# Performance work log

Hardware: AMD Instinct MI355X
Metric: run time of the kernel (lower is better)

Reference implementation:

```python
import jax, jax.numpy as jnp
import numpy as np

jax.config.update("jax_enable_x64", True)

QN = 20       # number of qubits -> statevector shape (2,)*QN, complex128 (16 MB)
LAYERS = 8    # circuit depth

# diagonal of CZ on a qubit pair, and the ZZ parity matrix for Rzz
_CZ_DIAG = np.array([[1.0, 1.0], [1.0, -1.0]], dtype=np.complex128)   # (-1)^{b1 b2}
_ZZ = np.array([[1.0, -1.0], [-1.0, 1.0]], dtype=np.float64)          # (-1)^{b1 xor b2}


def _apply_1q(psi, U, q):
    """Contract 2x2 gate U into leg q of the rank-QN state tensor."""
    psi = jnp.tensordot(U, psi, axes=([1], [q]))  # new leg at axis 0
    return jnp.moveaxis(psi, 0, q)


def _pair_shape(q):
    # broadcast shape putting a (2,2) factor on legs (q, q+1)
    return (1,) * q + (2, 2) + (1,) * (QN - q - 2)


def _layer(psi, theta_l, phi_l):
    """One circuit layer: Ry on every qubit, CZ chain, Rzz chain (transpiled CNOT/RZZ style)."""
    # single-qubit Ry(theta) gates (fixed small loop over qubits; each is a tiny contraction)
    for q in range(QN):
        c = jnp.cos(theta_l[q] * 0.5)
        s = jnp.sin(theta_l[q] * 0.5)
        U = jnp.stack([jnp.stack([c, -s]), jnp.stack([s, c])]).astype(jnp.complex128)
        psi = _apply_1q(psi, U, q)
    # CZ entangling chain (diagonal gate -> elementwise phase multiply)
    for q in range(QN - 1):
        psi = psi * jnp.asarray(_CZ_DIAG).reshape(_pair_shape(q))
    # Rzz(phi) chain: diag exp(-i*phi/2 * Z(x)Z), also a pure phase
    for q in range(QN - 1):
        d = jnp.exp((-0.5j) * phi_l[q].astype(jnp.float64) * jnp.asarray(_ZZ))
        psi = psi * d.reshape(_pair_shape(q))
    return psi


def setup_inputs() -> dict:
    key = jax.random.key(0)
    k1, k2 = jax.random.split(key)
    theta = jax.random.normal(k1, (LAYERS, QN), dtype=jnp.float32)
    phi = jax.random.normal(k2, (LAYERS, QN - 1), dtype=jnp.float32)
    return {"theta": theta, "phi": phi}


def reference(theta, phi):
    theta = theta.astype(jnp.float64)
    phi = phi.astype(jnp.float64)
    # initial |0...0> state, complex128 as in the torch module
    psi0 = jnp.zeros((2,) * QN, dtype=jnp.complex128).at[(0,) * QN].set(1.0)
    layer = jax.checkpoint(_layer)

    def step(psi, tp):
        th_l, ph_l = tp
        return layer(psi, th_l, ph_l), None

    psi, _ = jax.lax.scan(step, psi0, (theta, phi))
    # measurement probabilities over the full computational basis
    return (jnp.abs(psi) ** 2).reshape(-1)
```

## Files before the change

### kernel.cpp

```cpp
#include <hip/hip_runtime.h>


#define QN 20

__device__ __forceinline__ float2 cmulf(float2 a, float2 b) {
    return make_float2(a.x * b.x - a.y * b.y, a.x * b.y + a.y * b.x);
}

__device__ __forceinline__ void rot2c(float2& x0, float2& x1, float2 w) {
    float2 t0 = make_float2(w.x * x0.x - w.y * x1.x, w.x * x0.y - w.y * x1.y);
    float2 t1 = make_float2(w.y * x0.x + w.x * x1.x, w.y * x0.y + w.x * x1.y);
    x0 = t0; x1 = t1;
}
__device__ __forceinline__ void rot4c(float2& a0, float2& a1, float2& a2, float2& a3,
                                      float2 wa, float2 wb) {
    rot2c(a0, a1, wa); rot2c(a2, a3, wa);
    rot2c(a0, a2, wb); rot2c(a1, a3, wb);
}

template<int X>
__device__ __forceinline__ float2 xpart(float2 v, int t) {
    int sx = __float_as_int(v.x), sy = __float_as_int(v.y);
    if constexpr (X == 4) {
        int ax = __builtin_amdgcn_update_dpp(sx, sx, 0x114, 0xF, 0xF, false);
        int ay = __builtin_amdgcn_update_dpp(sy, sy, 0x114, 0xF, 0xF, false);
        int bx = __builtin_amdgcn_update_dpp(sx, sx, 0x104, 0xF, 0xF, false);
        int by = __builtin_amdgcn_update_dpp(sy, sy, 0x104, 0xF, 0xF, false);
        bool hi = (t & 4) != 0;
        return make_float2(__int_as_float(hi ? ax : bx), __int_as_float(hi ? ay : by));
    } else {
        constexpr int ctrl = (X == 1) ? 0xB1 : (X == 2) ? 0x4E : 0x128;
        return make_float2(
            __int_as_float(__builtin_amdgcn_update_dpp(sx, sx, ctrl, 0xF, 0xF, false)),
            __int_as_float(__builtin_amdgcn_update_dpp(sy, sy, ctrl, 0xF, 0xF, false)));
    }
}

template<int X>
__device__ __forceinline__ void lrot4(float2& a0, float2& a1, float2& a2, float2& a3,
                                      float2 w, int t) {
    float ss = (t & X) ? w.y : -w.y;
    float2 p0 = xpart<X>(a0, t), p1 = xpart<X>(a1, t),
           p2 = xpart<X>(a2, t), p3 = xpart<X>(a3, t);
    a0 = make_float2(fmaf(ss, p0.x, w.x * a0.x), fmaf(ss, p0.y, w.x * a0.y));
    a1 = make_float2(fmaf(ss, p1.x, w.x * a1.x), fmaf(ss, p1.y, w.x * a1.y));
    a2 = make_float2(fmaf(ss, p2.x, w.x * a2.x), fmaf(ss, p2.y, w.x * a2.y));
    a3 = make_float2(fmaf(ss, p3.x, w.x * a3.x), fmaf(ss, p3.y, w.x * a3.y));
}

__device__ __forceinline__ float2 dphase(int x, const float2* Plo, const float2* Phh) {
    int y = (x ^ (x >> 1)) & 0x7FFFF;
    float2 p = cmulf(Plo[y & 1023], Phh[y >> 10]);
    int sgn = (__popc(x & (x >> 1) & 0x7FFFF) & 1) << 31;
    p.x = __int_as_float(__float_as_int(p.x) ^ sgn);
    p.y = __int_as_float(__float_as_int(p.y) ^ sgn);
    return p;
}

__device__ __forceinline__ void build_D(float2* Plo, float2* Phh,
                                        const float* __restrict__ ph, int t) {
    float pw[19];
    #pragma unroll
    for (int j = 0; j < 19; ++j) pw[j] = ph[18 - j];
    float S = 0.f;
    #pragma unroll
    for (int j = 0; j < 19; ++j) S += pw[j];
    float ang = 0.f;
    #pragma unroll
    for (int j = 0; j < 10; ++j) if ((t >> j) & 1) ang += pw[j];
    Plo[t] = make_float2(cosf(ang), sinf(ang));
    if (t < 512) {
        float a2 = -0.5f * S;
        #pragma unroll
        for (int j = 0; j < 9; ++j) if ((t >> j) & 1) a2 += pw[10 + j];
        Phh[t] = make_float2(cosf(a2), sinf(a2));
    }
}

__device__ __forceinline__ void pass_w1(float2* buf, int t,
                                        float2 a0, float2 a1, float2 a2, float2 a3) {
    int mb = ((t >> 4) & 3) | (((t >> 6) & 0xF) << 2) |
             (((t >> 2) & 3) << 6) | ((t & 3) << 10);
    int pb = mb ^ ((t & 3) << 2) ^ (((t >> 2) & 3) << 4);
    buf[pb] = a0; buf[pb | 256] = a1; buf[pb | 512] = a2; buf[pb | 768] = a3;
}
__device__ __forceinline__ void pass_r1(const float2* buf, int t,
                                        float2& a0, float2& a1, float2& a2, float2& a3) {
    int rb = (4 * t) ^ (((t >> 8) & 3) << 2) ^ (((t >> 4) & 3) << 4);
    const float4* b4 = (const float4*)(buf + rb);
    float4 u = b4[0], w = b4[1];
    a0 = make_float2(u.x, u.y); a1 = make_float2(u.z, u.w);
    a2 = make_float2(w.x, w.y); a3 = make_float2(w.z, w.w);
}
__device__ __forceinline__ int q_nb(int t) {
    return ((t >> 6) & 0xF) | (((t >> 4) & 3) << 4) | ((t & 0xF) << 8);
}
__device__ __forceinline__ void pass_w2(float2* buf, int t,
                                        float2 a0, float2 a1, float2 a2, float2 a3) {
    int nb = q_nb(t);
    int qb = nb ^ (t & 3) ^ (((t >> 2) & 3) << 2);
    buf[qb] = a0; buf[qb ^ 0x50] = a1; buf[qb ^ 0xA0] = a2; buf[qb ^ 0xF0] = a3;
}
__device__ __forceinline__ void pass_r2(const float2* buf, int t,
                                        float2& a0, float2& a1, float2& a2, float2& a3) {
    int rb = (4 * t) ^ (((t >> 8) & 3) << 2) ^ (((t >> 4) & 3) << 4);
    const float4* b4 = (const float4*)(buf + rb);
    float4 u = b4[0], w = b4[1];
    float2 r0 = make_float2(u.x, u.y), r1 = make_float2(u.z, u.w),
           r2 = make_float2(w.x, w.y), r3 = make_float2(w.z, w.w);
    int k = (t >> 6) & 3;
    if (k & 1) { float2 x = r0; r0 = r1; r1 = x; x = r2; r2 = r3; r3 = x; }
    if (k & 2) { float2 x = r0; r0 = r2; r2 = x; x = r1; r1 = r3; r3 = x; }
    a0 = r0; a1 = r1; a2 = r2; a3 = r3;
}

__device__ __forceinline__ int hi_x(int n, int blk) {
    return ((n >> 3) << 11) | (blk << 3) | (n & 7);
}

template<bool LAST>
__global__ __launch_bounds__(1024)
void low_kernel(float2* __restrict__ psi, const float2* __restrict__ cA,
                const float2* __restrict__ cB, const float* __restrict__ ph,
                float* __restrict__ outP) {
    __shared__ __align__(16) float2 bufA[4096];
    __shared__ __align__(16) float2 bufB[4096];
    __shared__ float2 Plo[1024];
    __shared__ float2 Phh[512];
    const int t = threadIdx.x, blk = blockIdx.x;

    const float4* gp = (const float4*)(psi + (blk << 12));
    float4 v0 = gp[2 * t], v1 = gp[2 * t + 1];

    if (!LAST) build_D(Plo, Phh, ph, t);

    float2 a0 = make_float2(v0.x, v0.y), a1 = make_float2(v0.z, v0.w),
           a2 = make_float2(v1.x, v1.y), a3 = make_float2(v1.z, v1.w);

    rot4c(a0, a1, a2, a3, cA[0], cA[1]);
    lrot4<1>(a0, a1, a2, a3, cA[2], t);
    lrot4<2>(a0, a1, a2, a3, cA[3], t);
    lrot4<4>(a0, a1, a2, a3, cA[4], t);
    lrot4<8>(a0, a1, a2, a3, cA[5], t);

    pass_w1(bufA, t, a0, a1, a2, a3);
    __syncthreads();
    pass_r1(bufA, t, a0, a1, a2, a3);

    rot4c(a0, a1, a2, a3, cA[6], cA[7]);
    lrot4<1>(a0, a1, a2, a3, cA[8], t);
    lrot4<2>(a0, a1, a2, a3, cA[9], t);
    lrot4<4>(a0, a1, a2, a3, cA[10], t);

    int nb = q_nb(t);
    if (LAST) {
        float* bf = (float*)bufB;
        int qb = nb ^ (t & 3) ^ (((t >> 2) & 3) << 2);
        bf[qb]        = a0.x * a0.x + a0.y * a0.y;
        bf[qb ^ 0x50] = a1.x * a1.x + a1.y * a1.y;
        bf[qb ^ 0xA0] = a2.x * a2.x + a2.y * a2.y;
        bf[qb ^ 0xF0] = a3.x * a3.x + a3.y * a3.y;
        __syncthreads();
        int rb = (4 * t) ^ (((t >> 8) & 3) << 2) ^ (((t >> 4) & 3) << 4);
        float4 u = *(const float4*)(bf + rb);
        int k = (t >> 6) & 3;
        if (k & 1) { float x = u.x; u.x = u.y; u.y = x; x = u.z; u.z = u.w; u.w = x; }
        if (k & 2) { float x = u.x; u.x = u.z; u.z = x; x = u.y; u.y = u.w; u.w = x; }
        *(float4*)(outP + (blk << 12) + 4 * t) = u;
    } else {
        int xb = blk << 12;
        a0 = cmulf(a0, dphase(xb | nb,        Plo, Phh));
        a1 = cmulf(a1, dphase(xb | nb | 0x40, Plo, Phh));
        a2 = cmulf(a2, dphase(xb | nb | 0x80, Plo, Phh));
        a3 = cmulf(a3, dphase(xb | nb | 0xC0, Plo, Phh));
        rot4c(a0, a1, a2, a3, cB[6], cB[7]);
        lrot4<1>(a0, a1, a2, a3, cB[8], t);
        lrot4<2>(a0, a1, a2, a3, cB[9], t);
        lrot4<4>(a0, a1, a2, a3, cB[10], t);
        lrot4<8>(a0, a1, a2, a3, cB[11], t);

        pass_w2(bufB, t, a0, a1, a2, a3);
        __syncthreads();
        pass_r2(bufB, t, a0, a1, a2, a3);

        lrot4<1>(a0, a1, a2, a3, cB[2], t);
        lrot4<2>(a0, a1, a2, a3, cB[3], t);
        lrot4<4>(a0, a1, a2, a3, cB[4], t);
        lrot4<8>(a0, a1, a2, a3, cB[5], t);
        rot4c(a0, a1, a2, a3, cB[0], cB[1]);
        float4* op = (float4*)(psi + (blk << 12));
        op[2 * t]     = make_float4(a0.x, a0.y, a1.x, a1.y);
        op[2 * t + 1] = make_float4(a2.x, a2.y, a3.x, a3.y);
    }
}

__global__ __launch_bounds__(1024)
void hi_kernel(float2* __restrict__ psi, const float2* __restrict__ cA,
               const float2* __restrict__ cB, const float* __restrict__ ph) {
    __shared__ __align__(16) float2 bufA[4096];
    __shared__ __align__(16) float2 bufB[4096];
    __shared__ float2 Plo[1024];
    __shared__ float2 Phh[512];
    const int t = threadIdx.x, blk = blockIdx.x;
    const int ga = ((t >> 1) << 11) | (blk << 3) | ((t & 1) << 2);

    const float4* gp = (const float4*)(psi + ga);
    float4 v0 = gp[0], v1 = gp[1];

    build_D(Plo, Phh, ph, t);

    float2 a0 = make_float2(v0.x, v0.y), a1 = make_float2(v0.z, v0.w),
           a2 = make_float2(v1.x, v1.y), a3 = make_float2(v1.z, v1.w);

    lrot4<4>(a0, a1, a2, a3, cA[12], t);
    lrot4<8>(a0, a1, a2, a3, cA[13], t);

    pass_w1(bufA, t, a0, a1, a2, a3);
    __syncthreads();
    pass_r1(bufA, t, a0, a1, a2, a3);

    rot4c(a0, a1, a2, a3, cA[14], cA[15]);
    lrot4<1>(a0, a1, a2, a3, cA[16], t);
    lrot4<2>(a0, a1, a2, a3, cA[17], t);
    lrot4<4>(a0, a1, a2, a3, cA[18], t);
    lrot4<8>(a0, a1, a2, a3, cA[19], t);

    int nb = q_nb(t);
    a0 = cmulf(a0, dphase(hi_x(nb,        blk), Plo, Phh));
    a1 = cmulf(a1, dphase(hi_x(nb | 0x40, blk), Plo, Phh));
    a2 = cmulf(a2, dphase(hi_x(nb | 0x80, blk), Plo, Phh));
    a3 = cmulf(a3, dphase(hi_x(nb | 0xC0, blk), Plo, Phh));

    rot4c(a0, a1, a2, a3, cB[14], cB[15]);
    lrot4<1>(a0, a1, a2, a3, cB[16], t);
    lrot4<2>(a0, a1, a2, a3, cB[17], t);
    lrot4<4>(a0, a1, a2, a3, cB[18], t);
    lrot4<8>(a0, a1, a2, a3, cB[19], t);

    pass_w2(bufB, t, a0, a1, a2, a3);
    __syncthreads();
    pass_r2(bufB, t, a0, a1, a2, a3);

    lrot4<2>(a0, a1, a2, a3, cB[11], t);
    lrot4<4>(a0, a1, a2, a3, cB[12], t);
    lrot4<8>(a0, a1, a2, a3, cB[13], t);

    float4* gp2 = (float4*)(psi + ga);
    gp2[0] = make_float4(a0.x, a0.y, a1.x, a1.y);
    gp2[1] = make_float4(a2.x, a2.y, a3.x, a3.y);
}

__global__ __launch_bounds__(1024)
void init_kernel(float2* __restrict__ psi, const float* __restrict__ th,
                 const float* __restrict__ ph, float2* __restrict__ cw) {
    __shared__ __align__(16) float2 bufB[4096];
    __shared__ float2 Plo[1024];
    __shared__ float2 Phh[512];
    __shared__ float Alo[1024], Ahi[1024];
    __shared__ float2 cAi[20], cBi[20];
    const int t = threadIdx.x, blk = blockIdx.x;
    const int ga = ((t >> 1) << 11) | (blk << 3) | ((t & 1) << 2);

    if (t < 256) {
        int l = t >> 5, f = t & 31;
        if (f < 20) {
            double a = 0.5 * (double)th[l * 20 + 19 - f];
            float2 w = make_float2((float)cos(a), (float)sin(a));
            cw[l * 20 + f] = w;
            if (l == 0) cAi[f] = w;
            else if (l == 1) cBi[f] = w;
        }
    }
    __syncthreads();

    build_D(Plo, Phh, ph, t);
    {
        float pl = 1.f, ph2 = 1.f;
        #pragma unroll
        for (int j = 0; j < 10; ++j) {
            pl  *= ((t >> j) & 1) ? cAi[j].y      : cAi[j].x;
            ph2 *= ((t >> j) & 1) ? cAi[10 + j].y : cAi[10 + j].x;
        }
        Alo[t] = pl; Ahi[t] = ph2;
    }
    __syncthreads();

    int nb = q_nb(t);
    float2 a0, a1, a2, a3;
    {
        int x0 = hi_x(nb, blk),        x1 = hi_x(nb | 0x40, blk),
            x2 = hi_x(nb | 0x80, blk), x3 = hi_x(nb | 0xC0, blk);
        float m0 = Alo[x0 & 1023] * Ahi[x0 >> 10];
        float m1 = Alo[x1 & 1023] * Ahi[x1 >> 10];
        float m2 = Alo[x2 & 1023] * Ahi[x2 >> 10];
        float m3 = Alo[x3 & 1023] * Ahi[x3 >> 10];
        float2 d0 = dphase(x0, Plo, Phh), d1 = dphase(x1, Plo, Phh),
               d2 = dphase(x2, Plo, Phh), d3 = dphase(x3, Plo, Phh);
        a0 = make_float2(m0 * d0.x, m0 * d0.y);
        a1 = make_float2(m1 * d1.x, m1 * d1.y);
        a2 = make_float2(m2 * d2.x, m2 * d2.y);
        a3 = make_float2(m3 * d3.x, m3 * d3.y);
    }

    rot4c(a0, a1, a2, a3, cBi[14], cBi[15]);
    lrot4<1>(a0, a1, a2, a3, cBi[16], t);
    lrot4<2>(a0, a1, a2, a3, cBi[17], t);
    lrot4<4>(a0, a1, a2, a3, cBi[18], t);
    lrot4<8>(a0, a1, a2, a3, cBi[19], t);

    pass_w2(bufB, t, a0, a1, a2, a3);
    __syncthreads();
    pass_r2(bufB, t, a0, a1, a2, a3);

    lrot4<2>(a0, a1, a2, a3, cBi[11], t);
    lrot4<4>(a0, a1, a2, a3, cBi[12], t);
    lrot4<8>(a0, a1, a2, a3, cBi[13], t);

    float4* gp2 = (float4*)(psi + ga);
    gp2[0] = make_float4(a0.x, a0.y, a1.x, a1.y);
    gp2[1] = make_float4(a2.x, a2.y, a3.x, a3.y);
}

extern "C" void kernel_launch(void* const* d_in, const int* in_sizes, int n_in,
                              void* d_out, int out_size, void* d_ws, size_t ws_size,
                              hipStream_t stream) {
    (void)in_sizes; (void)n_in; (void)out_size; (void)ws_size;
    const float* th = (const float*)d_in[0];
    const float* ph = (const float*)d_in[1];
    float2* psi = (float2*)d_ws;
    float2* cw  = (float2*)((char*)d_ws + (8u << 20));
    float* out = (float*)d_out;

    init_kernel      <<<256, 1024, 0, stream>>>(psi, th, ph + 0, cw);
    low_kernel<false><<<256, 1024, 0, stream>>>(psi, cw + 1 * 20, cw + 2 * 20, ph +  19, nullptr);
    hi_kernel        <<<256, 1024, 0, stream>>>(psi, cw + 2 * 20, cw + 3 * 20, ph +  38);
    low_kernel<false><<<256, 1024, 0, stream>>>(psi, cw + 3 * 20, cw + 4 * 20, ph +  57, nullptr);
    hi_kernel        <<<256, 1024, 0, stream>>>(psi, cw + 4 * 20, cw + 5 * 20, ph +  76);
    low_kernel<false><<<256, 1024, 0, stream>>>(psi, cw + 5 * 20, cw + 6 * 20, ph +  95, nullptr);
    hi_kernel        <<<256, 1024, 0, stream>>>(psi, cw + 6 * 20, cw + 7 * 20, ph + 114);
    low_kernel<true ><<<256, 1024, 0, stream>>>(psi, cw + 7 * 20, cw + 7 * 20, ph + 133, out);
}
```

Measured before the change: 94.56 us.

## Fuse all layer sweeps into a persistent mega-kernel with grid barriers

Replaces the eight separate kernel launches with one persistent kernel of 256 blocks that runs every sweep in turn, with an atomic-counter grid barrier between sweeps. The next layer's phase table build_D is now computed at the end of the previous sweep, so it lands before the barrier wait instead of at the start of the next sweep. This removes per-launch overhead and the gaps between kernels, but adds a memset and spin-wait barriers. It also relies on all 256 blocks of 1024 threads being resident at once; if they are not, the barrier deadlocks.

Result: slower. 253.7 us (+168.3%).

```diff
diff --git a/kernel.cpp b/kernel.cpp
--- a/kernel.cpp
+++ b/kernel.cpp
@@ -2,6 +2,7 @@
 
 
 #define QN 20
+#define NBLK 256
 
 __device__ __forceinline__ float2 cmulf(float2 a, float2 b) {
     return make_float2(a.x * b.x - a.y * b.y, a.x * b.y + a.y * b.x);
@@ -118,21 +119,25 @@
     return ((n >> 3) << 11) | (blk << 3) | (n & 7);
 }
 
+__device__ __forceinline__ void gbar(unsigned* cnt, unsigned phase) {
+    __syncthreads();
+    if (threadIdx.x == 0) {
+        __threadfence();
+        atomicAdd(cnt, 1u);
+        const unsigned target = phase * (unsigned)NBLK;
+        while (atomicAdd(cnt, 0u) < target) __builtin_amdgcn_s_sleep(1);
+        __threadfence();
+    }
+    __syncthreads();
+}
+
 template<bool LAST>
-__global__ __launch_bounds__(1024)
-void low_kernel(float2* __restrict__ psi, const float2* __restrict__ cA,
-                const float2* __restrict__ cB, const float* __restrict__ ph,
-                float* __restrict__ outP) {
-    __shared__ __align__(16) float2 bufA[4096];
-    __shared__ __align__(16) float2 bufB[4096];
-    __shared__ float2 Plo[1024];
-    __shared__ float2 Phh[512];
-    const int t = threadIdx.x, blk = blockIdx.x;
-
+__device__ __forceinline__ void sweep_low(float2* __restrict__ psi,
+        const float2* cA, const float2* cB, const float* phN,
+        float* __restrict__ outP,
+        float2* bufA, float2* bufB, float2* Plo, float2* Phh, int t, int blk) {
     const float4* gp = (const float4*)(psi + (blk << 12));
     float4 v0 = gp[2 * t], v1 = gp[2 * t + 1];
-
-    if (!LAST) build_D(Plo, Phh, ph, t);
 
     float2 a0 = make_float2(v0.x, v0.y), a1 = make_float2(v0.z, v0.w),
            a2 = make_float2(v1.x, v1.y), a3 = make_float2(v1.z, v1.w);
@@ -191,23 +196,17 @@
         float4* op = (float4*)(psi + (blk << 12));
         op[2 * t]     = make_float4(a0.x, a0.y, a1.x, a1.y);
         op[2 * t + 1] = make_float4(a2.x, a2.y, a3.x, a3.y);
-    }
-}
-
-__global__ __launch_bounds__(1024)
-void hi_kernel(float2* __restrict__ psi, const float2* __restrict__ cA,
-               const float2* __restrict__ cB, const float* __restrict__ ph) {
-    __shared__ __align__(16) float2 bufA[4096];
-    __shared__ __align__(16) float2 bufB[4096];
-    __shared__ float2 Plo[1024];
-    __shared__ float2 Phh[512];
-    const int t = threadIdx.x, blk = blockIdx.x;
+        if (phN) build_D(Plo, Phh, phN, t);
+    }
+}
+
+__device__ __forceinline__ void sweep_hi(float2* __restrict__ psi,
+        const float2* cA, const float2* cB, const float* phN,
+        float2* bufA, float2* bufB, float2* Plo, float2* Phh, int t, int blk) {
     const int ga = ((t >> 1) << 11) | (blk << 3) | ((t & 1) << 2);
 
     const float4* gp = (const float4*)(psi + ga);
     float4 v0 = gp[0], v1 = gp[1];
-
-    build_D(Plo, Phh, ph, t);
 
     float2 a0 = make_float2(v0.x, v0.y), a1 = make_float2(v0.z, v0.w),
            a2 = make_float2(v1.x, v1.y), a3 = make_float2(v1.z, v1.w);
@@ -248,17 +247,17 @@
     float4* gp2 = (float4*)(psi + ga);
     gp2[0] = make_float4(a0.x, a0.y, a1.x, a1.y);
     gp2[1] = make_float4(a2.x, a2.y, a3.x, a3.y);
-}
-
-__global__ __launch_bounds__(1024)
-void init_kernel(float2* __restrict__ psi, const float* __restrict__ th,
-                 const float* __restrict__ ph, float2* __restrict__ cw) {
-    __shared__ __align__(16) float2 bufB[4096];
-    __shared__ float2 Plo[1024];
-    __shared__ float2 Phh[512];
-    __shared__ float Alo[1024], Ahi[1024];
-    __shared__ float2 cAi[20], cBi[20];
-    const int t = threadIdx.x, blk = blockIdx.x;
+    if (phN) build_D(Plo, Phh, phN, t);
+}
+
+__device__ __forceinline__ void sweep_init(float2* __restrict__ psi,
+        const float* __restrict__ th, const float* __restrict__ ph0,
+        const float* phN, float2* __restrict__ cw,
+        float2* bufA, float2* bufB, float2* Plo, float2* Phh, int t, int blk) {
+    float* Alo = (float*)bufA;
+    float* Ahi = Alo + 1024;
+    float2* cAi = bufA + 1024;
+    float2* cBi = bufA + 1056;
     const int ga = ((t >> 1) << 11) | (blk << 3) | ((t & 1) << 2);
 
     if (t < 256) {
@@ -273,7 +272,7 @@
     }
     __syncthreads();
 
-    build_D(Plo, Phh, ph, t);
+    build_D(Plo, Phh, ph0, t);
     {
         float pl = 1.f, ph2 = 1.f;
         #pragma unroll
@@ -319,6 +318,34 @@
     float4* gp2 = (float4*)(psi + ga);
     gp2[0] = make_float4(a0.x, a0.y, a1.x, a1.y);
     gp2[1] = make_float4(a2.x, a2.y, a3.x, a3.y);
+    if (phN) build_D(Plo, Phh, phN, t);
+}
+
+__global__ __launch_bounds__(1024)
+void mega_kernel(float2* __restrict__ psi, const float* __restrict__ th,
+                 const float* __restrict__ ph, float2* __restrict__ cw,
+                 float* __restrict__ outP, unsigned* __restrict__ bar) {
+    __shared__ __align__(16) float2 bufA[4096];
+    __shared__ __align__(16) float2 bufB[4096];
+    __shared__ float2 Plo[1024];
+    __shared__ float2 Phh[512];
+    const int t = threadIdx.x, blk = blockIdx.x;
+
+    sweep_init(psi, th, ph, ph + 19, cw, bufA, bufB, Plo, Phh, t, blk);
+    gbar(bar, 1);
+    sweep_low<false>(psi, cw + 20,  cw + 40,  ph + 38, nullptr, bufA, bufB, Plo, Phh, t, blk);
+    gbar(bar, 2);
+    sweep_hi        (psi, cw + 40,  cw + 60,  ph + 57,          bufA, bufB, Plo, Phh, t, blk);
+    gbar(bar, 3);
+    sweep_low<false>(psi, cw + 60,  cw + 80,  ph + 76, nullptr, bufA, bufB, Plo, Phh, t, blk);
+    gbar(bar, 4);
+    sweep_hi        (psi, cw + 80,  cw + 100, ph + 95,          bufA, bufB, Plo, Phh, t, blk);
+    gbar(bar, 5);
+    sweep_low<false>(psi, cw + 100, cw + 120, ph + 114, nullptr, bufA, bufB, Plo, Phh, t, blk);
+    gbar(bar, 6);
+    sweep_hi        (psi, cw + 120, cw + 140, nullptr,          bufA, bufB, Plo, Phh, t, blk);
+    gbar(bar, 7);
+    sweep_low<true> (psi, cw + 140, cw + 140, nullptr, outP,    bufA, bufB, Plo, Phh, t, blk);
 }
 
 extern "C" void kernel_launch(void* const* d_in, const int* in_sizes, int n_in,
@@ -329,14 +356,9 @@
     const float* ph = (const float*)d_in[1];
     float2* psi = (float2*)d_ws;
     float2* cw  = (float2*)((char*)d_ws + (8u << 20));
+    unsigned* bar = (unsigned*)((char*)d_ws + (8u << 20) + 4096);
     float* out = (float*)d_out;
 
-    init_kernel      <<<256, 1024, 0, stream>>>(psi, th, ph + 0, cw);
-    low_kernel<false><<<256, 1024, 0, stream>>>(psi, cw + 1 * 20, cw + 2 * 20, ph +  19, nullptr);
-    hi_kernel        <<<256, 1024, 0, stream>>>(psi, cw + 2 * 20, cw + 3 * 20, ph +  38);
-    low_kernel<false><<<256, 1024, 0, stream>>>(psi, cw + 3 * 20, cw + 4 * 20, ph +  57, nullptr);
-    hi_kernel        <<<256, 1024, 0, stream>>>(psi, cw + 4 * 20, cw + 5 * 20, ph +  76);
-    low_kernel<false><<<256, 1024, 0, stream>>>(psi, cw + 5 * 20, cw + 6 * 20, ph +  95, nullptr);
-    hi_kernel        <<<256, 1024, 0, stream>>>(psi, cw + 6 * 20, cw + 7 * 20, ph + 114);
-    low_kernel<true ><<<256, 1024, 0, stream>>>(psi, cw + 7 * 20, cw + 7 * 20, ph + 133, out);
-}
+    hipMemsetAsync(bar, 0, 64, stream);
+    mega_kernel<<<NBLK, 1024, 0, stream>>>(psi, th, ph, cw, out, bar);
+}
```

## Shrink blocks to 512 threads with 2048-amplitude tiles and rebalance qubit split

Applied to the files above, without the earlier changes.

Halves each block's tile from 4096 to 2048 amplitudes, using 512 threads and 512 blocks. This moves the low/high qubit split from 12/8 to 11/9 bits and rewrites the shared-memory transpose index maps and the high-qubit gather addressing to match. The aim is more resident blocks per CU, less LDS per block and better load balance across the 256 CUs. The cost is a reworked gate-to-pass assignment with new swizzles that must stay conflict-free and correct, and a build_D that now fills its tables in two iterations per thread.

New measurement: 84.53 us. 10.6% less time.

```diff
diff --git a/kernel.cpp b/kernel.cpp
--- a/kernel.cpp
+++ b/kernel.cpp
@@ -65,11 +65,15 @@
     float S = 0.f;
     #pragma unroll
     for (int j = 0; j < 19; ++j) S += pw[j];
-    float ang = 0.f;
     #pragma unroll
-    for (int j = 0; j < 10; ++j) if ((t >> j) & 1) ang += pw[j];
-    Plo[t] = make_float2(cosf(ang), sinf(ang));
-    if (t < 512) {
+    for (int k2 = 0; k2 < 2; ++k2) {
+        int i = t + (k2 << 9);
+        float ang = 0.f;
+        #pragma unroll
+        for (int j = 0; j < 10; ++j) if ((i >> j) & 1) ang += pw[j];
+        Plo[i] = make_float2(cosf(ang), sinf(ang));
+    }
+    {
         float a2 = -0.5f * S;
         #pragma unroll
         for (int j = 0; j < 9; ++j) if ((t >> j) & 1) a2 += pw[10 + j];
@@ -79,31 +83,30 @@
 
 __device__ __forceinline__ void pass_w1(float2* buf, int t,
                                         float2 a0, float2 a1, float2 a2, float2 a3) {
-    int mb = ((t >> 4) & 3) | (((t >> 6) & 0xF) << 2) |
-             (((t >> 2) & 3) << 6) | ((t & 3) << 10);
-    int pb = mb ^ ((t & 3) << 2) ^ (((t >> 2) & 3) << 4);
-    buf[pb] = a0; buf[pb | 256] = a1; buf[pb | 512] = a2; buf[pb | 768] = a3;
+    int mb = ((t >> 4) & 3) | (((t >> 6) & 7) << 2) |
+             (((t >> 1) & 7) << 5) | ((t & 1) << 10);
+    int pb = mb ^ (((t >> 1) & 7) << 2);
+    buf[pb] = a0; buf[pb | 0x100] = a1; buf[pb | 0x200] = a2; buf[pb | 0x300] = a3;
 }
 __device__ __forceinline__ void pass_r1(const float2* buf, int t,
                                         float2& a0, float2& a1, float2& a2, float2& a3) {
-    int rb = (4 * t) ^ (((t >> 8) & 3) << 2) ^ (((t >> 4) & 3) << 4);
+    int rb = (4 * t) ^ (((t >> 3) & 7) << 2);
     const float4* b4 = (const float4*)(buf + rb);
     float4 u = b4[0], w = b4[1];
     a0 = make_float2(u.x, u.y); a1 = make_float2(u.z, u.w);
     a2 = make_float2(w.x, w.y); a3 = make_float2(w.z, w.w);
 }
 __device__ __forceinline__ int q_nb(int t) {
-    return ((t >> 6) & 0xF) | (((t >> 4) & 3) << 4) | ((t & 0xF) << 8);
+    return ((t >> 6) & 7) | (((t >> 3) & 7) << 3) | ((t & 7) << 8);
 }
 __device__ __forceinline__ void pass_w2(float2* buf, int t,
                                         float2 a0, float2 a1, float2 a2, float2 a3) {
-    int nb = q_nb(t);
-    int qb = nb ^ (t & 3) ^ (((t >> 2) & 3) << 2);
-    buf[qb] = a0; buf[qb ^ 0x50] = a1; buf[qb ^ 0xA0] = a2; buf[qb ^ 0xF0] = a3;
+    int q0 = q_nb(t) ^ (t & 7);
+    buf[q0] = a0; buf[q0 | 0x40] = a1; buf[q0 | 0x80] = a2; buf[q0 | 0xC0] = a3;
 }
 __device__ __forceinline__ void pass_r2(const float2* buf, int t,
                                         float2& a0, float2& a1, float2& a2, float2& a3) {
-    int rb = (4 * t) ^ (((t >> 8) & 3) << 2) ^ (((t >> 4) & 3) << 4);
+    int rb = (4 * t) ^ (((t >> 8) & 1) << 2);
     const float4* b4 = (const float4*)(buf + rb);
     float4 u = b4[0], w = b4[1];
     float2 r0 = make_float2(u.x, u.y), r1 = make_float2(u.z, u.w),
@@ -114,22 +117,18 @@
     a0 = r0; a1 = r1; a2 = r2; a3 = r3;
 }
 
-__device__ __forceinline__ int hi_x(int n, int blk) {
-    return ((n >> 3) << 11) | (blk << 3) | (n & 7);
-}
-
 template<bool LAST>
-__global__ __launch_bounds__(1024)
+__global__ __launch_bounds__(512)
 void low_kernel(float2* __restrict__ psi, const float2* __restrict__ cA,
                 const float2* __restrict__ cB, const float* __restrict__ ph,
                 float* __restrict__ outP) {
-    __shared__ __align__(16) float2 bufA[4096];
-    __shared__ __align__(16) float2 bufB[4096];
+    __shared__ __align__(16) float2 bufA[2048];
+    __shared__ __align__(16) float2 bufB[2048];
     __shared__ float2 Plo[1024];
     __shared__ float2 Phh[512];
     const int t = threadIdx.x, blk = blockIdx.x;
 
-    const float4* gp = (const float4*)(psi + (blk << 12));
+    const float4* gp = (const float4*)(psi + (blk << 11));
     float4 v0 = gp[2 * t], v1 = gp[2 * t + 1];
 
     if (!LAST) build_D(Plo, Phh, ph, t);
@@ -155,29 +154,28 @@
     int nb = q_nb(t);
     if (LAST) {
         float* bf = (float*)bufB;
-        int qb = nb ^ (t & 3) ^ (((t >> 2) & 3) << 2);
-        bf[qb]        = a0.x * a0.x + a0.y * a0.y;
-        bf[qb ^ 0x50] = a1.x * a1.x + a1.y * a1.y;
-        bf[qb ^ 0xA0] = a2.x * a2.x + a2.y * a2.y;
-        bf[qb ^ 0xF0] = a3.x * a3.x + a3.y * a3.y;
+        int q0 = nb ^ (t & 7);
+        bf[q0]        = a0.x * a0.x + a0.y * a0.y;
+        bf[q0 | 0x40] = a1.x * a1.x + a1.y * a1.y;
+        bf[q0 | 0x80] = a2.x * a2.x + a2.y * a2.y;
+        bf[q0 | 0xC0] = a3.x * a3.x + a3.y * a3.y;
         __syncthreads();
-        int rb = (4 * t) ^ (((t >> 8) & 3) << 2) ^ (((t >> 4) & 3) << 4);
-        float4 u = *(const float4*)(bf + rb);
+        int rbf = (4 * t) ^ (((t >> 8) & 1) << 2);
+        float4 u = *(const float4*)(bf + rbf);
         int k = (t >> 6) & 3;
         if (k & 1) { float x = u.x; u.x = u.y; u.y = x; x = u.z; u.z = u.w; u.w = x; }
         if (k & 2) { float x = u.x; u.x = u.z; u.z = x; x = u.y; u.y = u.w; u.w = x; }
-        *(float4*)(outP + (blk << 12) + 4 * t) = u;
+        *(float4*)(outP + (blk << 11) + 4 * t) = u;
     } else {
-        int xb = blk << 12;
-        a0 = cmulf(a0, dphase(xb | nb,        Plo, Phh));
-        a1 = cmulf(a1, dphase(xb | nb | 0x40, Plo, Phh));
-        a2 = cmulf(a2, dphase(xb | nb | 0x80, Plo, Phh));
-        a3 = cmulf(a3, dphase(xb | nb | 0xC0, Plo, Phh));
+        int xb = blk << 11;
+        a0 = cmulf(a0, dphase(xb | nb,            Plo, Phh));
+        a1 = cmulf(a1, dphase(xb | nb | (1 << 6), Plo, Phh));
+        a2 = cmulf(a2, dphase(xb | nb | (2 << 6), Plo, Phh));
+        a3 = cmulf(a3, dphase(xb | nb | (3 << 6), Plo, Phh));
         rot4c(a0, a1, a2, a3, cB[6], cB[7]);
         lrot4<1>(a0, a1, a2, a3, cB[8], t);
         lrot4<2>(a0, a1, a2, a3, cB[9], t);
         lrot4<4>(a0, a1, a2, a3, cB[10], t);
-        lrot4<8>(a0, a1, a2, a3, cB[11], t);
 
         pass_w2(bufB, t, a0, a1, a2, a3);
         __syncthreads();
@@ -188,21 +186,22 @@
         lrot4<4>(a0, a1, a2, a3, cB[4], t);
         lrot4<8>(a0, a1, a2, a3, cB[5], t);
         rot4c(a0, a1, a2, a3, cB[0], cB[1]);
-        float4* op = (float4*)(psi + (blk << 12));
+        float4* op = (float4*)(psi + (blk << 11));
         op[2 * t]     = make_float4(a0.x, a0.y, a1.x, a1.y);
         op[2 * t + 1] = make_float4(a2.x, a2.y, a3.x, a3.y);
     }
 }
 
-__global__ __launch_bounds__(1024)
+__global__ __launch_bounds__(512)
 void hi_kernel(float2* __restrict__ psi, const float2* __restrict__ cA,
                const float2* __restrict__ cB, const float* __restrict__ ph) {
-    __shared__ __align__(16) float2 bufA[4096];
-    __shared__ __align__(16) float2 bufB[4096];
+    __shared__ __align__(16) float2 bufA[2048];
+    __shared__ __align__(16) float2 bufB[2048];
     __shared__ float2 Plo[1024];
     __shared__ float2 Phh[512];
     const int t = threadIdx.x, blk = blockIdx.x;
-    const int ga = ((t >> 1) << 11) | (blk << 3) | ((t & 1) << 2);
+    const int cid = ((blk >> 7) & 3) | ((blk & 0x7F) << 2);
+    const int ga = (cid << 2) | ((t & 63) << 11) | (((t >> 6) & 7) << 17);
 
     const float4* gp = (const float4*)(psi + ga);
     float4 v0 = gp[0], v1 = gp[1];
@@ -212,54 +211,60 @@
     float2 a0 = make_float2(v0.x, v0.y), a1 = make_float2(v0.z, v0.w),
            a2 = make_float2(v1.x, v1.y), a3 = make_float2(v1.z, v1.w);
 
-    lrot4<4>(a0, a1, a2, a3, cA[12], t);
-    lrot4<8>(a0, a1, a2, a3, cA[13], t);
+    lrot4<1>(a0, a1, a2, a3, cA[11], t);
+    lrot4<2>(a0, a1, a2, a3, cA[12], t);
+    lrot4<4>(a0, a1, a2, a3, cA[13], t);
+    lrot4<8>(a0, a1, a2, a3, cA[14], t);
 
     pass_w1(bufA, t, a0, a1, a2, a3);
     __syncthreads();
     pass_r1(bufA, t, a0, a1, a2, a3);
 
-    rot4c(a0, a1, a2, a3, cA[14], cA[15]);
-    lrot4<1>(a0, a1, a2, a3, cA[16], t);
-    lrot4<2>(a0, a1, a2, a3, cA[17], t);
-    lrot4<4>(a0, a1, a2, a3, cA[18], t);
-    lrot4<8>(a0, a1, a2, a3, cA[19], t);
-
-    int nb = q_nb(t);
-    a0 = cmulf(a0, dphase(hi_x(nb,        blk), Plo, Phh));
-    a1 = cmulf(a1, dphase(hi_x(nb | 0x40, blk), Plo, Phh));
-    a2 = cmulf(a2, dphase(hi_x(nb | 0x80, blk), Plo, Phh));
-    a3 = cmulf(a3, dphase(hi_x(nb | 0xC0, blk), Plo, Phh));
-
-    rot4c(a0, a1, a2, a3, cB[14], cB[15]);
-    lrot4<1>(a0, a1, a2, a3, cB[16], t);
-    lrot4<2>(a0, a1, a2, a3, cB[17], t);
-    lrot4<4>(a0, a1, a2, a3, cB[18], t);
-    lrot4<8>(a0, a1, a2, a3, cB[19], t);
+    rot4c(a0, a1, a2, a3, cA[15], cA[16]);
+    lrot4<1>(a0, a1, a2, a3, cA[17], t);
+    lrot4<2>(a0, a1, a2, a3, cA[18], t);
+    lrot4<4>(a0, a1, a2, a3, cA[19], t);
+
+    int mb = q_nb(t);
+    int xbase = (mb & 3) | (cid << 2) | ((mb >> 2) << 11);
+    a0 = cmulf(a0, dphase(xbase,             Plo, Phh));
+    a1 = cmulf(a1, dphase(xbase | (1 << 15), Plo, Phh));
+    a2 = cmulf(a2, dphase(xbase | (2 << 15), Plo, Phh));
+    a3 = cmulf(a3, dphase(xbase | (3 << 15), Plo, Phh));
+
+    rot4c(a0, a1, a2, a3, cB[15], cB[16]);
+    lrot4<1>(a0, a1, a2, a3, cB[17], t);
+    lrot4<2>(a0, a1, a2, a3, cB[18], t);
+    lrot4<4>(a0, a1, a2, a3, cB[19], t);
 
     pass_w2(bufB, t, a0, a1, a2, a3);
     __syncthreads();
     pass_r2(bufB, t, a0, a1, a2, a3);
 
-    lrot4<2>(a0, a1, a2, a3, cB[11], t);
-    lrot4<4>(a0, a1, a2, a3, cB[12], t);
-    lrot4<8>(a0, a1, a2, a3, cB[13], t);
+    lrot4<1>(a0, a1, a2, a3, cB[11], t);
+    lrot4<2>(a0, a1, a2, a3, cB[12], t);
+    lrot4<4>(a0, a1, a2, a3, cB[13], t);
+    lrot4<8>(a0, a1, a2, a3, cB[14], t);
 
     float4* gp2 = (float4*)(psi + ga);
     gp2[0] = make_float4(a0.x, a0.y, a1.x, a1.y);
     gp2[1] = make_float4(a2.x, a2.y, a3.x, a3.y);
 }
 
-__global__ __launch_bounds__(1024)
+__global__ __launch_bounds__(512)
 void init_kernel(float2* __restrict__ psi, const float* __restrict__ th,
                  const float* __restrict__ ph, float2* __restrict__ cw) {
-    __shared__ __align__(16) float2 bufB[4096];
+    __shared__ __align__(16) float2 bufA[2048];
+    __shared__ __align__(16) float2 bufB[2048];
     __shared__ float2 Plo[1024];
     __shared__ float2 Phh[512];
-    __shared__ float Alo[1024], Ahi[1024];
-    __shared__ float2 cAi[20], cBi[20];
+    float* Alo = (float*)bufA;
+    float* Ahi = Alo + 1024;
+    float2* cAi = bufA + 1024;
+    float2* cBi = bufA + 1056;
     const int t = threadIdx.x, blk = blockIdx.x;
-    const int ga = ((t >> 1) << 11) | (blk << 3) | ((t & 1) << 2);
+    const int cid = ((blk >> 7) & 3) | ((blk & 0x7F) << 2);
+    const int ga = (cid << 2) | ((t & 63) << 11) | (((t >> 6) & 7) << 17);
 
     if (t < 256) {
         int l = t >> 5, f = t & 31;
@@ -274,22 +279,25 @@
     __syncthreads();
 
     build_D(Plo, Phh, ph, t);
-    {
+    #pragma unroll
+    for (int k2 = 0; k2 < 2; ++k2) {
+        int i = t + (k2 << 9);
         float pl = 1.f, ph2 = 1.f;
         #pragma unroll
         for (int j = 0; j < 10; ++j) {
-            pl  *= ((t >> j) & 1) ? cAi[j].y      : cAi[j].x;
-            ph2 *= ((t >> j) & 1) ? cAi[10 + j].y : cAi[10 + j].x;
+            pl  *= ((i >> j) & 1) ? cAi[j].y      : cAi[j].x;
+            ph2 *= ((i >> j) & 1) ? cAi[10 + j].y : cAi[10 + j].x;
         }
-        Alo[t] = pl; Ahi[t] = ph2;
-    }
-    __syncthreads();
-
-    int nb = q_nb(t);
+        Alo[i] = pl; Ahi[i] = ph2;
+    }
+    __syncthreads();
+
+    int mb = q_nb(t);
+    int xbase = (mb & 3) | (cid << 2) | ((mb >> 2) << 11);
     float2 a0, a1, a2, a3;
     {
-        int x0 = hi_x(nb, blk),        x1 = hi_x(nb | 0x40, blk),
-            x2 = hi_x(nb | 0x80, blk), x3 = hi_x(nb | 0xC0, blk);
+        int x0 = xbase,             x1 = xbase | (1 << 15),
+            x2 = xbase | (2 << 15), x3 = xbase | (3 << 15);
         float m0 = Alo[x0 & 1023] * Ahi[x0 >> 10];
         float m1 = Alo[x1 & 1023] * Ahi[x1 >> 10];
         float m2 = Alo[x2 & 1023] * Ahi[x2 >> 10];
@@ -302,19 +310,19 @@
         a3 = make_float2(m3 * d3.x, m3 * d3.y);
     }
 
-    rot4c(a0, a1, a2, a3, cBi[14], cBi[15]);
-    lrot4<1>(a0, a1, a2, a3, cBi[16], t);
-    lrot4<2>(a0, a1, a2, a3, cBi[17], t);
-    lrot4<4>(a0, a1, a2, a3, cBi[18], t);
-    lrot4<8>(a0, a1, a2, a3, cBi[19], t);
+    rot4c(a0, a1, a2, a3, cBi[15], cBi[16]);
+    lrot4<1>(a0, a1, a2, a3, cBi[17], t);
+    lrot4<2>(a0, a1, a2, a3, cBi[18], t);
+    lrot4<4>(a0, a1, a2, a3, cBi[19], t);
 
     pass_w2(bufB, t, a0, a1, a2, a3);
     __syncthreads();
     pass_r2(bufB, t, a0, a1, a2, a3);
 
-    lrot4<2>(a0, a1, a2, a3, cBi[11], t);
-    lrot4<4>(a0, a1, a2, a3, cBi[12], t);
-    lrot4<8>(a0, a1, a2, a3, cBi[13], t);
+    lrot4<1>(a0, a1, a2, a3, cBi[11], t);
+    lrot4<2>(a0, a1, a2, a3, cBi[12], t);
+    lrot4<4>(a0, a1, a2, a3, cBi[13], t);
+    lrot4<8>(a0, a1, a2, a3, cBi[14], t);
 
     float4* gp2 = (float4*)(psi + ga);
     gp2[0] = make_float4(a0.x, a0.y, a1.x, a1.y);
@@ -331,12 +339,12 @@
     float2* cw  = (float2*)((char*)d_ws + (8u << 20));
     float* out = (float*)d_out;
 
-    init_kernel      <<<256, 1024, 0, stream>>>(psi, th, ph + 0, cw);
-    low_kernel<false><<<256, 1024, 0, stream>>>(psi, cw + 1 * 20, cw + 2 * 20, ph +  19, nullptr);
-    hi_kernel        <<<256, 1024, 0, stream>>>(psi, cw + 2 * 20, cw + 3 * 20, ph +  38);
-    low_kernel<false><<<256, 1024, 0, stream>>>(psi, cw + 3 * 20, cw + 4 * 20, ph +  57, nullptr);
-    hi_kernel        <<<256, 1024, 0, stream>>>(psi, cw + 4 * 20, cw + 5 * 20, ph +  76);
-    low_kernel<false><<<256, 1024, 0, stream>>>(psi, cw + 5 * 20, cw + 6 * 20, ph +  95, nullptr);
-    hi_kernel        <<<256, 1024, 0, stream>>>(psi, cw + 6 * 20, cw + 7 * 20, ph + 114);
-    low_kernel<true ><<<256, 1024, 0, stream>>>(psi, cw + 7 * 20, cw + 7 * 20, ph + 133, out);
-}
+    init_kernel      <<<512, 512, 0, stream>>>(psi, th, ph, cw);
+    low_kernel<false><<<512, 512, 0, stream>>>(psi, cw + 1 * 20, cw + 2 * 20, ph +  19, nullptr);
+    hi_kernel        <<<512, 512, 0, stream>>>(psi, cw + 2 * 20, cw + 3 * 20, ph +  38);
+    low_kernel<false><<<512, 512, 0, stream>>>(psi, cw + 3 * 20, cw + 4 * 20, ph +  57, nullptr);
+    hi_kernel        <<<512, 512, 0, stream>>>(psi, cw + 4 * 20, cw + 5 * 20, ph +  76);
+    low_kernel<false><<<512, 512, 0, stream>>>(psi, cw + 5 * 20, cw + 6 * 20, ph +  95, nullptr);
+    hi_kernel        <<<512, 512, 0, stream>>>(psi, cw + 6 * 20, cw + 7 * 20, ph + 114);
+    low_kernel<true ><<<512, 512, 0, stream>>>(psi, cw + 7 * 20, cw + 7 * 20, ph + 133, out);
+}
```
